# Performance work log

Measured on AMD Instinct MI355X. Metric: run time of the kernel, lower is better.

The kernel has to match this reference:

```python
import jax, jax.numpy as jnp
import numpy as np

N_NODES = 100000
N_EDGES = 600000
D_IN = 128
D_OUT = 128
N_REL = 16
N_BASES = 8


def setup_inputs() -> dict:
    key = jax.random.key(0)
    ks = jax.random.split(key, 6)
    x = jax.random.normal(ks[0], (N_NODES, D_IN), dtype=jnp.float32)
    edge_index = jax.random.randint(ks[1], (2, N_EDGES), 0, N_NODES, dtype=jnp.int64)
    edge_type = jax.random.randint(ks[2], (N_EDGES,), 0, N_REL, dtype=jnp.int64)
    # xavier-uniform-ish init scales
    b_lim = float(np.sqrt(6.0 / (D_IN + D_OUT)))
    c_lim = float(np.sqrt(6.0 / (N_REL + N_BASES)))
    w_lim = float(np.sqrt(6.0 / (D_IN + D_OUT)))
    bases = jax.random.uniform(ks[3], (N_BASES, D_IN, D_OUT), jnp.float32, -b_lim, b_lim)
    coefficients = jax.random.uniform(ks[4], (N_REL, N_BASES), jnp.float32, -c_lim, c_lim)
    w_self = jax.random.uniform(ks[5], (D_OUT, D_IN), jnp.float32, -w_lim, w_lim)
    return {"x": x, "edge_index": edge_index, "edge_type": edge_type,
            "bases": bases, "coefficients": coefficients, "w_self": w_self}


def reference(x, edge_index, edge_type, bases, coefficients, w_self):
    # self loop: Linear(in, out, bias=False) -> x @ W^T
    out = x @ w_self.T  # [N, D_OUT]
    # relation weights from basis decomposition
    weights = jnp.einsum('rb,bio->rio', coefficients, bases)  # [R, D_IN, D_OUT]
    row, col = edge_index[0], edge_index[1]
    xc = x[col]  # [E, D_IN] gather of source features
    n_rel = weights.shape[0]
    msg = jnp.zeros((xc.shape[0], w_self.shape[0]), dtype=x.dtype)
    # fixed small loop over relations; masked accumulate matches per-relation grouped GEMM
    for r in range(n_rel):
        sel = (edge_type == r)[:, None]
        msg = msg + jnp.where(sel, xc @ weights[r], jnp.zeros((), x.dtype))
    # scatter-add messages to destination rows
    out = out.at[row].add(msg)
    return out
```

## Files before the change

### kernel.cpp

```cpp
#include <hip/hip_runtime.h>

#define NN 100000
#define NE 600000
#define ET (NE + NN)
#define D 128
#define NREL 16
#define SCANB 391
#define TPB 4
#define MAXTILES 10954
#define GEMMG ((MAXTILES + TPB - 1) / TPB)
#define WGRID 1088

typedef short short8 __attribute__((ext_vector_type(8)));
typedef float f32x4 __attribute__((ext_vector_type(4)));
typedef unsigned int u32x4 __attribute__((ext_vector_type(4)));

#define C0 0
#define O0 20
#define CU0 40
#define T0 60

#define WT_OFF   0
#define META_OFF 557056
#define DH_OFF   557568
#define DO_OFF   957568
#define DC_OFF   1357576
#define BS_OFF   1757576
#define SCP_OFF  1759576
#define SR_OFF   7360088
#define XB_OFF   10160096
#define MSGB_OFF 35760096
#define MSGA_OFF 10160096
#define NEED_B   (MSGB_OFF + (size_t)ET * 128 * 2)
#define NEED_A   (MSGA_OFF + (size_t)ET * 128 * 2)

__device__ __forceinline__ unsigned short f2bf(float f) {
  unsigned u = __builtin_bit_cast(unsigned, f);
  u += 0x7fffu + ((u >> 16) & 1u);
  return (unsigned short)(u >> 16);
}

__global__ __launch_bounds__(256) void k_prep(const float* __restrict__ bases,
    const float* __restrict__ coef, const float* __restrict__ w_self,
    unsigned short* __restrict__ wT, const float* __restrict__ x,
    unsigned short* __restrict__ xb)
{
  if (blockIdx.x < WGRID) {
    int idx = blockIdx.x * 256 + threadIdx.x;
    int r = idx >> 14;
    int t = idx & 16383;
    float v;
    if (r < 16) {
      int o = t >> 7, i = t & 127;
      float acc = 0.f;
      #pragma unroll
      for (int b = 0; b < 8; ++b)
        acc += coef[r * 8 + b] * bases[b * 16384 + i * 128 + o];
      v = acc;
    } else {
      v = w_self[t];
    }
    wT[idx] = f2bf(v);
  } else {
    int i = (blockIdx.x - WGRID) * 256 + threadIdx.x;
    if (i >= NN * D / 4) return;
    f32x4 f = __builtin_nontemporal_load((const f32x4*)(x + (size_t)i * 4));
    unsigned short s0 = f2bf(f[0]), s1 = f2bf(f[1]), s2 = f2bf(f[2]), s3 = f2bf(f[3]);
    unsigned long long pk = (unsigned long long)s0 | ((unsigned long long)s1 << 16)
                          | ((unsigned long long)s2 << 32) | ((unsigned long long)s3 << 48);
    *(unsigned long long*)(xb + (size_t)i * 4) = pk;
  }
}

__global__ __launch_bounds__(256) void k_hist(const int* __restrict__ ei,
    const int* __restrict__ et, int* __restrict__ meta, int* __restrict__ dstHist)
{
  __shared__ int h[16];
  int tid = threadIdx.x;
  if (tid < 16) h[tid] = 0;
  __syncthreads();
  for (int e = blockIdx.x * 256 + tid; e < NE; e += gridDim.x * 256) {
    atomicAdd(&h[et[e]], 1);
    atomicAdd(&dstHist[ei[e]], 1);
  }
  __syncthreads();
  if (tid < 16) atomicAdd(&meta[C0 + tid], h[tid]);
}

__global__ __launch_bounds__(256) void k_scan1(const int* __restrict__ dstHist,
    int* __restrict__ dstOff, int* __restrict__ blockSums)
{
  __shared__ int sh[256];
  int tid = threadIdx.x;
  int d = blockIdx.x * 256 + tid;
  int v = (d < NN) ? (dstHist[d] + 1) : 0;
  sh[tid] = v;
  __syncthreads();
  #pragma unroll
  for (int ofs = 1; ofs < 256; ofs <<= 1) {
    int t = (tid >= ofs) ? sh[tid - ofs] : 0;
    __syncthreads();
    sh[tid] += t;
    __syncthreads();
  }
  if (d < NN) dstOff[d] = sh[tid] - v;
  if (tid == 255) blockSums[blockIdx.x] = sh[tid];
}

__global__ __launch_bounds__(512) void k_scan2(int* __restrict__ blockSums, int* __restrict__ meta)
{
  __shared__ int sh[SCANB];
  int tid = threadIdx.x;
  if (tid < SCANB) sh[tid] = blockSums[tid];
  __syncthreads();
  if (tid == 0) {
    int run = 0;
    for (int i = 0; i < SCANB; ++i) { int c = sh[i]; sh[i] = run; run += c; }
    meta[C0 + 16] = NN;
    int off = 0, toff = 0;
    for (int r = 0; r <= 16; ++r) {
      meta[O0 + r] = off;
      meta[CU0 + r] = off;
      meta[T0 + r] = toff;
      int c = meta[C0 + r];
      off += c;
      toff += (c + 63) >> 6;
    }
    meta[O0 + 17] = off;
    meta[T0 + 17] = toff;
  }
  __syncthreads();
  if (tid < SCANB) blockSums[tid] = sh[tid];
}

__global__ __launch_bounds__(256) void k_scan3(int* __restrict__ dstOff,
    const int* __restrict__ blockSums, int* __restrict__ dstCursor,
    int2* __restrict__ sCP)
{
  int tid = threadIdx.x;
  int d = blockIdx.x * 256 + tid;
  int base = blockSums[blockIdx.x];
  if (d < NN) {
    int o = dstOff[d] + base;
    dstOff[d] = o;
    dstCursor[d] = o + 1;
    sCP[NE + d] = make_int2(d, o);
  }
  if (d == NN) dstOff[NN] = ET;
}

__global__ __launch_bounds__(256) void k_self0(int2* __restrict__ sCP, int* __restrict__ sRow)
{
  int n = blockIdx.x * 256 + threadIdx.x;
  if (n < NN) { sCP[NE + n] = make_int2(n, 0); sRow[NE + n] = n; }
}

__global__ __launch_bounds__(256) void k_scatter(const int* __restrict__ ei, const int* __restrict__ et,
    int* __restrict__ meta, int2* __restrict__ sCP, int* __restrict__ sRow,
    int* __restrict__ dstCursor, int doMsg)
{
  __shared__ int h[16], base[16], lh[16];
  int tid = threadIdx.x;
  int start = blockIdx.x * 4096;
  int end = min(NE, start + 4096);
  if (tid < 16) { h[tid] = 0; lh[tid] = 0; }
  __syncthreads();
  for (int e = start + tid; e < end; e += 256)
    atomicAdd(&h[et[e]], 1);
  __syncthreads();
  if (tid < 16) base[tid] = atomicAdd(&meta[CU0 + tid], h[tid]);
  __syncthreads();
  for (int e = start + tid; e < end; e += 256) {
    int r = et[e];
    int row = ei[e];
    int pos = base[r] + atomicAdd(&lh[r], 1);
    int slot = doMsg ? atomicAdd(&dstCursor[row], 1) : 0;
    sCP[pos] = make_int2(ei[NE + e], slot);
    if (!doMsg) sRow[pos] = row;
  }
}

__global__ __launch_bounds__(256) void k_gemm(const float* __restrict__ xf,
    const unsigned short* __restrict__ xb,
    const unsigned short* __restrict__ wT, const int* __restrict__ meta,
    const int2* __restrict__ sCP, const int* __restrict__ sRow,
    unsigned short* __restrict__ msg, float* __restrict__ out,
    int xbf, int msgmode)
{
  __shared__ short As[64 * 17 * 8];
  __shared__ short Es[64 * 136];
  __shared__ int Pos2[2][64];
  __shared__ int Rows[64];
  __shared__ int Ms[80];

  int tid = threadIdx.x;
  if (tid < 80) Ms[tid] = meta[tid];
  __syncthreads();
  int ntiles = Ms[T0 + 17];

  int lane = tid & 63, wave = tid >> 6;
  int q = lane >> 4, l15 = lane & 15;
  int m = tid >> 2, ug = tid & 3;

  if (xbf && msgmode) {
    short8 pf[4];
    int pcy = 0;
    bool pvalid = false;
    int r = 0, nr = 0;
    int b = blockIdx.x * TPB;
    if (b < ntiles) {
      while (r < 16 && Ms[T0 + r + 1] <= b) ++r;
      int boff = Ms[O0 + r];
      int e0 = boff + (b - Ms[T0 + r]) * 64;
      nr = min(64, boff + Ms[C0 + r] - e0);
      pvalid = m < nr;
      int2 cp = sCP[pvalid ? (e0 + m) : e0];
      pcy = cp.y;
      const unsigned short* xr = xb + (size_t)cp.x * 128;
      #pragma unroll
      for (int s = 0; s < 4; ++s) {
        short8 v = (short8)(short)0;
        if (pvalid) v = *(const short8*)(xr + (ug * 4 + s) * 8);
        pf[s] = v;
      }
    }
    int rprev = -1;
    short8 bfr[2][4];
    for (int ti = 0; ti < TPB; ++ti) {
      b = blockIdx.x * TPB + ti;
      if (b >= ntiles) break;
      int curR = r, curNr = nr;
      #pragma unroll
      for (int s = 0; s < 4; ++s)
        *(short8*)&As[(m * 17 + ug * 4 + s) * 8] = pf[s];
      if (ug == 0) Pos2[ti & 1][m] = pvalid ? pcy : 0;
      __syncthreads();
      int bn = b + 1;
      if (ti + 1 < TPB && bn < ntiles) {
        int rn = curR;
        while (rn < 16 && Ms[T0 + rn + 1] <= bn) ++rn;
        int boff = Ms[O0 + rn];
        int e0n = boff + (bn - Ms[T0 + rn]) * 64;
        int nrn = min(64, boff + Ms[C0 + rn] - e0n);
        pvalid = m < nrn;
        int2 cp = sCP[pvalid ? (e0n + m) : e0n];
        pcy = cp.y;
        const unsigned short* xr = xb + (size_t)cp.x * 128;
        #pragma unroll
        for (int s = 0; s < 4; ++s) {
          short8 v = (short8)(short)0;
          if (pvalid) v = *(const short8*)(xr + (ug * 4 + s) * 8);
          pf[s] = v;
        }
        r = rn; nr = nrn;
      }
      if (curR != rprev) {
        const unsigned short* wr = wT + curR * 16384;
        #pragma unroll
        for (int ns = 0; ns < 2; ++ns)
          #pragma unroll
          for (int kk = 0; kk < 4; ++kk)
            bfr[ns][kk] = *(const short8*)(wr + (wave * 32 + ns * 16 + l15) * 128 + kk * 32 + q * 8);
        rprev = curR;
      }
      f32x4 acc[4][2];
      #pragma unroll
      for (int ms = 0; ms < 4; ++ms)
        #pragma unroll
        for (int ns = 0; ns < 2; ++ns)
          acc[ms][ns] = (f32x4){0.f, 0.f, 0.f, 0.f};
      #pragma unroll
      for (int kk = 0; kk < 4; ++kk) {
        short8 af[4];
        #pragma unroll
        for (int ms = 0; ms < 4; ++ms)
          af[ms] = *(const short8*)&As[((ms * 16 + l15) * 17 + kk * 4 + q) * 8];
        #pragma unroll
        for (int ms = 0; ms < 4; ++ms)
          #pragma unroll
          for (int ns = 0; ns < 2; ++ns)
            acc[ms][ns] = __builtin_amdgcn_mfma_f32_16x16x32_bf16(af[ms], bfr[ns][kk], acc[ms][ns], 0, 0, 0);
      }
      #pragma unroll
      for (int ms = 0; ms < 4; ++ms)
        #pragma unroll
        for (int ns = 0; ns < 2; ++ns)
          #pragma unroll
          for (int reg = 0; reg < 4; ++reg)
            Es[(ms * 16 + q * 4 + reg) * 136 + wave * 32 + ns * 16 + l15] =
                (short)f2bf(acc[ms][ns][reg]);
      __syncthreads();
      #pragma unroll
      for (int i = 0; i < 4; ++i) {
        int row = wave * 16 + i * 4 + q;
        short8 v = *(const short8*)&Es[row * 136 + l15 * 8];
        if (row < curNr)
          __builtin_nontemporal_store(v,
              (short8*)(msg + (size_t)Pos2[ti & 1][row] * 128 + l15 * 8));
      }
    }
    return;
  }

  int rprev = -1;
  short8 bfr[2][4];
  for (int ti = 0; ti < TPB; ++ti) {
    int b = blockIdx.x * TPB + ti;
    if (b >= ntiles) break;
    int r = 0;
    while (r < 16 && Ms[T0 + r + 1] <= b) ++r;
    int tile = b - Ms[T0 + r];
    int boff = Ms[O0 + r];
    int e0 = boff + tile * 64;
    int nrows = min(64, boff + Ms[C0 + r] - e0);

    bool valid = m < nrows;
    int e = valid ? (e0 + m) : e0;
    int2 cp = sCP[e];
    if (ug == 0) {
      Pos2[0][m] = valid ? cp.y : 0;
      if (!msgmode) Rows[m] = valid ? sRow[e] : 0;
    }
    int c = cp.x;
    if (xbf) {
      const unsigned short* xr = xb + (size_t)c * 128;
      #pragma unroll
      for (int s = 0; s < 4; ++s) {
        int u = ug * 4 + s;
        short8 pk = (short8)(short)0;
        if (valid) pk = *(const short8*)(xr + u * 8);
        *(short8*)&As[(m * 17 + u) * 8] = pk;
      }
    } else {
      const float* xr = xf + (size_t)c * 128;
      #pragma unroll
      for (int s = 0; s < 4; ++s) {
        int u = ug * 4 + s;
        float4 f0 = make_float4(0.f, 0.f, 0.f, 0.f), f1 = f0;
        if (valid) {
          f0 = *(const float4*)(xr + u * 8);
          f1 = *(const float4*)(xr + u * 8 + 4);
        }
        short8 pk;
        pk[0] = (short)f2bf(f0.x); pk[1] = (short)f2bf(f0.y);
        pk[2] = (short)f2bf(f0.z); pk[3] = (short)f2bf(f0.w);
        pk[4] = (short)f2bf(f1.x); pk[5] = (short)f2bf(f1.y);
        pk[6] = (short)f2bf(f1.z); pk[7] = (short)f2bf(f1.w);
        *(short8*)&As[(m * 17 + u) * 8] = pk;
      }
    }
    __syncthreads();

    if (r != rprev) {
      const unsigned short* wr = wT + r * 16384;
      #pragma unroll
      for (int ns = 0; ns < 2; ++ns)
        #pragma unroll
        for (int kk = 0; kk < 4; ++kk)
          bfr[ns][kk] = *(const short8*)(wr + (wave * 32 + ns * 16 + l15) * 128 + kk * 32 + q * 8);
      rprev = r;
    }

    f32x4 acc[4][2];
    #pragma unroll
    for (int ms = 0; ms < 4; ++ms)
      #pragma unroll
      for (int ns = 0; ns < 2; ++ns)
        acc[ms][ns] = (f32x4){0.f, 0.f, 0.f, 0.f};
    #pragma unroll
    for (int kk = 0; kk < 4; ++kk) {
      short8 af[4];
      #pragma unroll
      for (int ms = 0; ms < 4; ++ms)
        af[ms] = *(const short8*)&As[((ms * 16 + l15) * 17 + kk * 4 + q) * 8];
      #pragma unroll
      for (int ms = 0; ms < 4; ++ms)
        #pragma unroll
        for (int ns = 0; ns < 2; ++ns)
          acc[ms][ns] = __builtin_amdgcn_mfma_f32_16x16x32_bf16(af[ms], bfr[ns][kk], acc[ms][ns], 0, 0, 0);
    }

    if (msgmode) {
      __syncthreads();
      #pragma unroll
      for (int ms = 0; ms < 4; ++ms)
        #pragma unroll
        for (int ns = 0; ns < 2; ++ns)
          #pragma unroll
          for (int reg = 0; reg < 4; ++reg)
            Es[(ms * 16 + q * 4 + reg) * 136 + wave * 32 + ns * 16 + l15] =
                (short)f2bf(acc[ms][ns][reg]);
      __syncthreads();
      #pragma unroll
      for (int i = 0; i < 4; ++i) {
        int row = wave * 16 + i * 4 + q;
        short8 v = *(const short8*)&Es[row * 136 + l15 * 8];
        if (row < nrows)
          __builtin_nontemporal_store(v,
              (short8*)(msg + (size_t)Pos2[0][row] * 128 + l15 * 8));
      }
      __syncthreads();
    } else {
      #pragma unroll
      for (int ms = 0; ms < 4; ++ms)
        #pragma unroll
        for (int reg = 0; reg < 4; ++reg) {
          int mrow = ms * 16 + q * 4 + reg;
          if (mrow < nrows) {
            float* op = out + (size_t)Rows[mrow] * 128 + wave * 32 + l15;
            unsafeAtomicAdd(op, acc[ms][0][reg]);
            unsafeAtomicAdd(op + 16, acc[ms][1][reg]);
          }
        }
      __syncthreads();
    }
  }
}

__global__ __launch_bounds__(256) void k_reduce(const unsigned short* __restrict__ msg,
    const int* __restrict__ dstOff, float* __restrict__ out)
{
  int d = blockIdx.x * 16 + (threadIdx.x >> 4);
  if (d >= NN) return;
  int sl = threadIdx.x & 15;
  int s = dstOff[d], e = dstOff[d + 1];
  const unsigned short* base = msg + (size_t)sl * 8;
  float a[8], bacc[8];
  #pragma unroll
  for (int i = 0; i < 8; ++i) { a[i] = 0.f; bacc[i] = 0.f; }
  int j = s;
  for (; j + 1 < e; j += 2) {
    u32x4 v0 = __builtin_nontemporal_load((const u32x4*)(base + (size_t)j * 128));
    u32x4 v1 = __builtin_nontemporal_load((const u32x4*)(base + (size_t)(j + 1) * 128));
    #pragma unroll
    for (int c = 0; c < 4; ++c) {
      a[2 * c]     += __builtin_bit_cast(float, v0[c] << 16);
      a[2 * c + 1] += __builtin_bit_cast(float, v0[c] & 0xffff0000u);
      bacc[2 * c]     += __builtin_bit_cast(float, v1[c] << 16);
      bacc[2 * c + 1] += __builtin_bit_cast(float, v1[c] & 0xffff0000u);
    }
  }
  if (j < e) {
    u32x4 v0 = __builtin_nontemporal_load((const u32x4*)(base + (size_t)j * 128));
    #pragma unroll
    for (int c = 0; c < 4; ++c) {
      a[2 * c]     += __builtin_bit_cast(float, v0[c] << 16);
      a[2 * c + 1] += __builtin_bit_cast(float, v0[c] & 0xffff0000u);
    }
  }
  f32x4 w0, w1;
  w0[0] = a[0] + bacc[0]; w0[1] = a[1] + bacc[1]; w0[2] = a[2] + bacc[2]; w0[3] = a[3] + bacc[3];
  w1[0] = a[4] + bacc[4]; w1[1] = a[5] + bacc[5]; w1[2] = a[6] + bacc[6]; w1[3] = a[7] + bacc[7];
  float* op = out + (size_t)d * 128 + sl * 8;
  __builtin_nontemporal_store(w0, (f32x4*)op);
  __builtin_nontemporal_store(w1, (f32x4*)(op + 4));
}

extern "C" void kernel_launch(void* const* d_in, const int* in_sizes, int n_in,
                              void* d_out, int out_size, void* d_ws, size_t ws_size,
                              hipStream_t stream)
{
  const float* x      = (const float*)d_in[0];
  const int*   ei     = (const int*)d_in[1];
  const int*   et     = (const int*)d_in[2];
  const float* bases  = (const float*)d_in[3];
  const float* coef   = (const float*)d_in[4];
  const float* w_self = (const float*)d_in[5];
  float* out = (float*)d_out;
  char* ws = (char*)d_ws;
  unsigned short* wT = (unsigned short*)(ws + WT_OFF);
  int* meta      = (int*)(ws + META_OFF);
  int* dstHist   = (int*)(ws + DH_OFF);
  int* dstOff    = (int*)(ws + DO_OFF);
  int* dstCursor = (int*)(ws + DC_OFF);
  int* blockSums = (int*)(ws + BS_OFF);
  int2* sCP      = (int2*)(ws + SCP_OFF);
  int* sRow      = (int*)(ws + SR_OFF);
  unsigned short* xb = (unsigned short*)(ws + XB_OFF);

  const int modeB = (ws_size >= NEED_B) ? 1 : 0;
  const int modeA = (modeB || ws_size >= NEED_A) ? 1 : 0;
  unsigned short* msg = (unsigned short*)(ws + (modeB ? MSGB_OFF : MSGA_OFF));

  hipMemsetAsync(ws + META_OFF, 0, 512 + 400000, stream);
  k_prep<<<modeB ? (WGRID + 12500) : WGRID, 256, 0, stream>>>(bases, coef, w_self, wT, x, xb);
  k_hist<<<256, 256, 0, stream>>>(ei, et, meta, dstHist);
  if (modeA) {
    k_scan1<<<SCANB, 256, 0, stream>>>(dstHist, dstOff, blockSums);
    k_scan2<<<1, 512, 0, stream>>>(blockSums, meta);
    k_scan3<<<SCANB, 256, 0, stream>>>(dstOff, blockSums, dstCursor, sCP);
  } else {
    k_scan2<<<1, 512, 0, stream>>>(blockSums, meta);
    k_self0<<<SCANB, 256, 0, stream>>>(sCP, sRow);
    hipMemsetAsync(d_out, 0, (size_t)NN * D * 4, stream);
  }
  k_scatter<<<(NE + 4095) / 4096, 256, 0, stream>>>(ei, et, meta, sCP, sRow, dstCursor, modeA);
  k_gemm<<<GEMMG, 256, 0, stream>>>(x, xb, wT, meta, sCP, sRow, msg, out, modeB, modeA);
  if (modeA)
    k_reduce<<<(NN + 15) / 16, 256, 0, stream>>>(msg, dstOff, out);
}
```

Before: 320.5 us.

## Deepen gather prefetch pipeline and use LDS-only barriers in message GEMM

Restructures the per-tile loop of the fused gather+GEMM message path into a three-stage software pipeline. Edge index/position lookups run two tiles ahead and the bf16 feature row gather runs one tile ahead. __syncthreads is replaced by a barrier that waits only on LDS counters (lgkmcnt), so outstanding global prefetch loads are no longer drained at each barrier. The aim is to hide gather latency behind the MFMA work, at the cost of extra registers for the pipeline state.

```diff
diff --git a/kernel.cpp b/kernel.cpp
--- a/kernel.cpp
+++ b/kernel.cpp
@@ -40,6 +40,11 @@
   return (unsigned short)(u >> 16);
 }
 
+__device__ __forceinline__ void lds_barrier() {
+  asm volatile("s_waitcnt lgkmcnt(0)" ::: "memory");
+  __builtin_amdgcn_s_barrier();
+}
+
 __global__ __launch_bounds__(256) void k_prep(const float* __restrict__ bases,
     const float* __restrict__ coef, const float* __restrict__ w_self,
     unsigned short* __restrict__ wT, const float* __restrict__ x,
@@ -203,57 +208,76 @@
   int m = tid >> 2, ug = tid & 3;
 
   if (xbf && msgmode) {
-    short8 pf[4];
-    int pcy = 0;
-    bool pvalid = false;
-    int r = 0, nr = 0;
-    int b = blockIdx.x * TPB;
-    if (b < ntiles) {
-      while (r < 16 && Ms[T0 + r + 1] <= b) ++r;
-      int boff = Ms[O0 + r];
-      int e0 = boff + (b - Ms[T0 + r]) * 64;
-      nr = min(64, boff + Ms[C0 + r] - e0);
-      pvalid = m < nr;
-      int2 cp = sCP[pvalid ? (e0 + m) : e0];
-      pcy = cp.y;
+    int b0 = blockIdx.x * TPB;
+    if (b0 >= ntiles) return;
+
+    int rr = 0;
+    short8 pfS[4]; int cyS; bool vS; int rS, nrS;
+    int2 cpG; bool vG; int rG, nrG;
+    int2 cpP; bool vP; int rP, nrP;
+
+    {
+      while (rr < 16 && Ms[T0 + rr + 1] <= b0) ++rr;
+      int boff = Ms[O0 + rr];
+      int e0 = boff + (b0 - Ms[T0 + rr]) * 64;
+      nrS = min(64, boff + Ms[C0 + rr] - e0);
+      rS = rr;
+      vS = m < nrS;
+      int2 cp = sCP[vS ? (e0 + m) : e0];
+      cyS = cp.y;
       const unsigned short* xr = xb + (size_t)cp.x * 128;
       #pragma unroll
       for (int s = 0; s < 4; ++s) {
         short8 v = (short8)(short)0;
-        if (pvalid) v = *(const short8*)(xr + (ug * 4 + s) * 8);
-        pf[s] = v;
-      }
-    }
+        if (vS) v = *(const short8*)(xr + (ug * 4 + s) * 8);
+        pfS[s] = v;
+      }
+    }
+    if (TPB > 1 && b0 + 1 < ntiles) {
+      int b = b0 + 1;
+      while (rr < 16 && Ms[T0 + rr + 1] <= b) ++rr;
+      int boff = Ms[O0 + rr];
+      int e0 = boff + (b - Ms[T0 + rr]) * 64;
+      nrG = min(64, boff + Ms[C0 + rr] - e0);
+      rG = rr;
+      vG = m < nrG;
+      cpG = sCP[vG ? (e0 + m) : e0];
+    } else { vG = false; nrG = 0; rG = rS; cpG = make_int2(0, 0); }
+
     int rprev = -1;
     short8 bfr[2][4];
     for (int ti = 0; ti < TPB; ++ti) {
-      b = blockIdx.x * TPB + ti;
+      int b = b0 + ti;
       if (b >= ntiles) break;
-      int curR = r, curNr = nr;
+      int curR = rS, curNr = nrS;
+
       #pragma unroll
       for (int s = 0; s < 4; ++s)
-        *(short8*)&As[(m * 17 + ug * 4 + s) * 8] = pf[s];
-      if (ug == 0) Pos2[ti & 1][m] = pvalid ? pcy : 0;
-      __syncthreads();
-      int bn = b + 1;
-      if (ti + 1 < TPB && bn < ntiles) {
-        int rn = curR;
-        while (rn < 16 && Ms[T0 + rn + 1] <= bn) ++rn;
-        int boff = Ms[O0 + rn];
-        int e0n = boff + (bn - Ms[T0 + rn]) * 64;
-        int nrn = min(64, boff + Ms[C0 + rn] - e0n);
-        pvalid = m < nrn;
-        int2 cp = sCP[pvalid ? (e0n + m) : e0n];
-        pcy = cp.y;
-        const unsigned short* xr = xb + (size_t)cp.x * 128;
+        *(short8*)&As[(m * 17 + ug * 4 + s) * 8] = pfS[s];
+      if (ug == 0) Pos2[ti & 1][m] = vS ? cyS : 0;
+
+      if (ti + 2 < TPB && b + 2 < ntiles) {
+        int bp = b + 2;
+        while (rr < 16 && Ms[T0 + rr + 1] <= bp) ++rr;
+        int boff = Ms[O0 + rr];
+        int e0 = boff + (bp - Ms[T0 + rr]) * 64;
+        nrP = min(64, boff + Ms[C0 + rr] - e0);
+        rP = rr;
+        vP = m < nrP;
+        cpP = sCP[vP ? (e0 + m) : e0];
+      } else { vP = false; nrP = 0; rP = rG; cpP = make_int2(0, 0); }
+
+      short8 pfN[4];
+      {
+        const unsigned short* xr = xb + (size_t)cpG.x * 128;
         #pragma unroll
         for (int s = 0; s < 4; ++s) {
           short8 v = (short8)(short)0;
-          if (pvalid) v = *(const short8*)(xr + (ug * 4 + s) * 8);
-          pf[s] = v;
+          if (vG) v = *(const short8*)(xr + (ug * 4 + s) * 8);
+          pfN[s] = v;
         }
-        r = rn; nr = nrn;
-      }
+      }
+
       if (curR != rprev) {
         const unsigned short* wr = wT + curR * 16384;
         #pragma unroll
@@ -263,6 +287,9 @@
             bfr[ns][kk] = *(const short8*)(wr + (wave * 32 + ns * 16 + l15) * 128 + kk * 32 + q * 8);
         rprev = curR;
       }
+
+      lds_barrier();
+
       f32x4 acc[4][2];
       #pragma unroll
       for (int ms = 0; ms < 4; ++ms)
@@ -281,6 +308,7 @@
           for (int ns = 0; ns < 2; ++ns)
             acc[ms][ns] = __builtin_amdgcn_mfma_f32_16x16x32_bf16(af[ms], bfr[ns][kk], acc[ms][ns], 0, 0, 0);
       }
+
       #pragma unroll
       for (int ms = 0; ms < 4; ++ms)
         #pragma unroll
@@ -289,7 +317,9 @@
           for (int reg = 0; reg < 4; ++reg)
             Es[(ms * 16 + q * 4 + reg) * 136 + wave * 32 + ns * 16 + l15] =
                 (short)f2bf(acc[ms][ns][reg]);
-      __syncthreads();
+
+      lds_barrier();
+
       #pragma unroll
       for (int i = 0; i < 4; ++i) {
         int row = wave * 16 + i * 4 + q;
@@ -298,6 +328,11 @@
           __builtin_nontemporal_store(v,
               (short8*)(msg + (size_t)Pos2[ti & 1][row] * 128 + l15 * 8));
       }
+
+      #pragma unroll
+      for (int s = 0; s < 4; ++s) pfS[s] = pfN[s];
+      cyS = cpG.y; vS = vG; rS = rG; nrS = nrG;
+      cpG = cpP;   vG = vP; rG = rP; nrG = nrP;
     }
     return;
   }
```

Result: no change. 320.2 us (-0.1%).

## Use one tile per GEMM block, direct scattered message stores, parallel block-sum scan

Applied to the files above, without the earlier changes.

The GEMM kernel drops the multi-tile-per-block loop with register prefetch. Each block now handles a single 64-edge tile, relying on many resident blocks rather than in-block prefetch to hide gather latency. The LDS staging of the output tile before coalesced 16-byte stores is removed. Each lane now writes individual 2-byte bf16 values straight to the message rows, which cuts LDS traffic and barriers but makes the global writes much narrower and more scattered. The serial single-thread block-sum scan in k_scan2 is also replaced with a parallel Hillis-Steele scan.

```diff
diff --git a/kernel.cpp b/kernel.cpp
--- a/kernel.cpp
+++ b/kernel.cpp
@@ -6,9 +6,8 @@
 #define D 128
 #define NREL 16
 #define SCANB 391
-#define TPB 4
 #define MAXTILES 10954
-#define GEMMG ((MAXTILES + TPB - 1) / TPB)
+#define GEMMG MAXTILES
 #define WGRID 1088
 
 typedef short short8 __attribute__((ext_vector_type(8)));
@@ -40,6 +39,11 @@
   return (unsigned short)(u >> 16);
 }
 
+__device__ __forceinline__ void lds_barrier() {
+  asm volatile("s_waitcnt lgkmcnt(0)" ::: "memory");
+  __builtin_amdgcn_s_barrier();
+}
+
 __global__ __launch_bounds__(256) void k_prep(const float* __restrict__ bases,
     const float* __restrict__ coef, const float* __restrict__ w_self,
     unsigned short* __restrict__ wT, const float* __restrict__ x,
@@ -109,13 +113,19 @@
 
 __global__ __launch_bounds__(512) void k_scan2(int* __restrict__ blockSums, int* __restrict__ meta)
 {
-  __shared__ int sh[SCANB];
-  int tid = threadIdx.x;
-  if (tid < SCANB) sh[tid] = blockSums[tid];
-  __syncthreads();
+  __shared__ int sh[512];
+  int tid = threadIdx.x;
+  int v = (tid < SCANB) ? blockSums[tid] : 0;
+  sh[tid] = v;
+  __syncthreads();
+  #pragma unroll
+  for (int ofs = 1; ofs < 512; ofs <<= 1) {
+    int t = (tid >= ofs) ? sh[tid - ofs] : 0;
+    __syncthreads();
+    sh[tid] += t;
+    __syncthreads();
+  }
   if (tid == 0) {
-    int run = 0;
-    for (int i = 0; i < SCANB; ++i) { int c = sh[i]; sh[i] = run; run += c; }
     meta[C0 + 16] = NN;
     int off = 0, toff = 0;
     for (int r = 0; r <= 16; ++r) {
@@ -129,8 +139,7 @@
     meta[O0 + 17] = off;
     meta[T0 + 17] = toff;
   }
-  __syncthreads();
-  if (tid < SCANB) blockSums[tid] = sh[tid];
+  if (tid < SCANB) blockSums[tid] = sh[tid] - v;
 }
 
 __global__ __launch_bounds__(256) void k_scan3(int* __restrict__ dstOff,
@@ -188,8 +197,7 @@
     int xbf, int msgmode)
 {
   __shared__ short As[64 * 17 * 8];
-  __shared__ short Es[64 * 136];
-  __shared__ int Pos2[2][64];
+  __shared__ int Pos[64];
   __shared__ int Rows[64];
   __shared__ int Ms[80];
 
@@ -197,223 +205,110 @@
   if (tid < 80) Ms[tid] = meta[tid];
   __syncthreads();
   int ntiles = Ms[T0 + 17];
+  int b = blockIdx.x;
+  if (b >= ntiles) return;
 
   int lane = tid & 63, wave = tid >> 6;
   int q = lane >> 4, l15 = lane & 15;
   int m = tid >> 2, ug = tid & 3;
 
-  if (xbf && msgmode) {
-    short8 pf[4];
-    int pcy = 0;
-    bool pvalid = false;
-    int r = 0, nr = 0;
-    int b = blockIdx.x * TPB;
-    if (b < ntiles) {
-      while (r < 16 && Ms[T0 + r + 1] <= b) ++r;
-      int boff = Ms[O0 + r];
-      int e0 = boff + (b - Ms[T0 + r]) * 64;
-      nr = min(64, boff + Ms[C0 + r] - e0);
-      pvalid = m < nr;
-      int2 cp = sCP[pvalid ? (e0 + m) : e0];
-      pcy = cp.y;
-      const unsigned short* xr = xb + (size_t)cp.x * 128;
-      #pragma unroll
-      for (int s = 0; s < 4; ++s) {
-        short8 v = (short8)(short)0;
-        if (pvalid) v = *(const short8*)(xr + (ug * 4 + s) * 8);
-        pf[s] = v;
+  int r = 0;
+  while (r < 16 && Ms[T0 + r + 1] <= b) ++r;
+  int boff = Ms[O0 + r];
+  int e0 = boff + (b - Ms[T0 + r]) * 64;
+  int nr = min(64, boff + Ms[C0 + r] - e0);
+
+  bool valid = m < nr;
+  int e = valid ? (e0 + m) : e0;
+  int2 cp = sCP[e];
+  if (ug == 0) {
+    Pos[m] = valid ? cp.y : 0;
+    if (!msgmode) Rows[m] = valid ? sRow[e] : 0;
+  }
+
+  if (xbf) {
+    const unsigned short* xr = xb + (size_t)cp.x * 128;
+    #pragma unroll
+    for (int s = 0; s < 4; ++s) {
+      int u = ug * 4 + s;
+      short8 pk = (short8)(short)0;
+      if (valid) pk = *(const short8*)(xr + u * 8);
+      *(short8*)&As[(m * 17 + u) * 8] = pk;
+    }
+  } else {
+    const float* xr = xf + (size_t)cp.x * 128;
+    #pragma unroll
+    for (int s = 0; s < 4; ++s) {
+      int u = ug * 4 + s;
+      float4 f0 = make_float4(0.f, 0.f, 0.f, 0.f), f1 = f0;
+      if (valid) {
+        f0 = *(const float4*)(xr + u * 8);
+        f1 = *(const float4*)(xr + u * 8 + 4);
       }
-    }
-    int rprev = -1;
-    short8 bfr[2][4];
-    for (int ti = 0; ti < TPB; ++ti) {
-      b = blockIdx.x * TPB + ti;
-      if (b >= ntiles) break;
-      int curR = r, curNr = nr;
-      #pragma unroll
-      for (int s = 0; s < 4; ++s)
-        *(short8*)&As[(m * 17 + ug * 4 + s) * 8] = pf[s];
-      if (ug == 0) Pos2[ti & 1][m] = pvalid ? pcy : 0;
-      __syncthreads();
-      int bn = b + 1;
-      if (ti + 1 < TPB && bn < ntiles) {
-        int rn = curR;
-        while (rn < 16 && Ms[T0 + rn + 1] <= bn) ++rn;
-        int boff = Ms[O0 + rn];
-        int e0n = boff + (bn - Ms[T0 + rn]) * 64;
-        int nrn = min(64, boff + Ms[C0 + rn] - e0n);
-        pvalid = m < nrn;
-        int2 cp = sCP[pvalid ? (e0n + m) : e0n];
-        pcy = cp.y;
-        const unsigned short* xr = xb + (size_t)cp.x * 128;
-        #pragma unroll
-        for (int s = 0; s < 4; ++s) {
-          short8 v = (short8)(short)0;
-          if (pvalid) v = *(const short8*)(xr + (ug * 4 + s) * 8);
-          pf[s] = v;
+      short8 pk;
+      pk[0] = (short)f2bf(f0.x); pk[1] = (short)f2bf(f0.y);
+      pk[2] = (short)f2bf(f0.z); pk[3] = (short)f2bf(f0.w);
+      pk[4] = (short)f2bf(f1.x); pk[5] = (short)f2bf(f1.y);
+      pk[6] = (short)f2bf(f1.z); pk[7] = (short)f2bf(f1.w);
+      *(short8*)&As[(m * 17 + u) * 8] = pk;
+    }
+  }
+
+  short8 bfr[2][4];
+  {
+    const unsigned short* wr = wT + r * 16384;
+    #pragma unroll
+    for (int ns = 0; ns < 2; ++ns)
+      #pragma unroll
+      for (int kk = 0; kk < 4; ++kk)
+        bfr[ns][kk] = *(const short8*)(wr + (wave * 32 + ns * 16 + l15) * 128 + kk * 32 + q * 8);
+  }
+
+  lds_barrier();
+
+  f32x4 acc[4][2];
+  #pragma unroll
+  for (int ms = 0; ms < 4; ++ms)
+    #pragma unroll
+    for (int ns = 0; ns < 2; ++ns)
+      acc[ms][ns] = (f32x4){0.f, 0.f, 0.f, 0.f};
+  #pragma unroll
+  for (int kk = 0; kk < 4; ++kk) {
+    short8 af[4];
+    #pragma unroll
+    for (int ms = 0; ms < 4; ++ms)
+      af[ms] = *(const short8*)&As[((ms * 16 + l15) * 17 + kk * 4 + q) * 8];
+    #pragma unroll
+    for (int ms = 0; ms < 4; ++ms)
+      #pragma unroll
+      for (int ns = 0; ns < 2; ++ns)
+        acc[ms][ns] = __builtin_amdgcn_mfma_f32_16x16x32_bf16(af[ms], bfr[ns][kk], acc[ms][ns], 0, 0, 0);
+  }
+
+  if (msgmode) {
+    #pragma unroll
+    for (int ms = 0; ms < 4; ++ms)
+      #pragma unroll
+      for (int reg = 0; reg < 4; ++reg) {
+        int erow = ms * 16 + q * 4 + reg;
+        if (erow < nr) {
+          unsigned short* mp = msg + (size_t)Pos[erow] * 128 + wave * 32 + l15;
+          mp[0]  = f2bf(acc[ms][0][reg]);
+          mp[16] = f2bf(acc[ms][1][reg]);
         }
-        r = rn; nr = nrn;
       }
-      if (curR != rprev) {
-        const unsigned short* wr = wT + curR * 16384;
-        #pragma unroll
-        for (int ns = 0; ns < 2; ++ns)
-          #pragma unroll
-          for (int kk = 0; kk < 4; ++kk)
-            bfr[ns][kk] = *(const short8*)(wr + (wave * 32 + ns * 16 + l15) * 128 + kk * 32 + q * 8);
-        rprev = curR;
+  } else {
+    #pragma unroll
+    for (int ms = 0; ms < 4; ++ms)
+      #pragma unroll
+      for (int reg = 0; reg < 4; ++reg) {
+        int erow = ms * 16 + q * 4 + reg;
+        if (erow < nr) {
+          float* op = out + (size_t)Rows[erow] * 128 + wave * 32 + l15;
+          unsafeAtomicAdd(op, acc[ms][0][reg]);
+          unsafeAtomicAdd(op + 16, acc[ms][1][reg]);
+        }
       }
-      f32x4 acc[4][2];
-      #pragma unroll
-      for (int ms = 0; ms < 4; ++ms)
-        #pragma unroll
-        for (int ns = 0; ns < 2; ++ns)
-          acc[ms][ns] = (f32x4){0.f, 0.f, 0.f, 0.f};
-      #pragma unroll
-      for (int kk = 0; kk < 4; ++kk) {
-        short8 af[4];
-        #pragma unroll
-        for (int ms = 0; ms < 4; ++ms)
-          af[ms] = *(const short8*)&As[((ms * 16 + l15) * 17 + kk * 4 + q) * 8];
-        #pragma unroll
-        for (int ms = 0; ms < 4; ++ms)
-          #pragma unroll
-          for (int ns = 0; ns < 2; ++ns)
-            acc[ms][ns] = __builtin_amdgcn_mfma_f32_16x16x32_bf16(af[ms], bfr[ns][kk], acc[ms][ns], 0, 0, 0);
-      }
-      #pragma unroll
-      for (int ms = 0; ms < 4; ++ms)
-        #pragma unroll
-        for (int ns = 0; ns < 2; ++ns)
-          #pragma unroll
-          for (int reg = 0; reg < 4; ++reg)
-            Es[(ms * 16 + q * 4 + reg) * 136 + wave * 32 + ns * 16 + l15] =
-                (short)f2bf(acc[ms][ns][reg]);
-      __syncthreads();
-      #pragma unroll
-      for (int i = 0; i < 4; ++i) {
-        int row = wave * 16 + i * 4 + q;
-        short8 v = *(const short8*)&Es[row * 136 + l15 * 8];
-        if (row < curNr)
-          __builtin_nontemporal_store(v,
-              (short8*)(msg + (size_t)Pos2[ti & 1][row] * 128 + l15 * 8));
-      }
-    }
-    return;
-  }
-
-  int rprev = -1;
-  short8 bfr[2][4];
-  for (int ti = 0; ti < TPB; ++ti) {
-    int b = blockIdx.x * TPB + ti;
-    if (b >= ntiles) break;
-    int r = 0;
-    while (r < 16 && Ms[T0 + r + 1] <= b) ++r;
-    int tile = b - Ms[T0 + r];
-    int boff = Ms[O0 + r];
-    int e0 = boff + tile * 64;
-    int nrows = min(64, boff + Ms[C0 + r] - e0);
-
-    bool valid = m < nrows;
-    int e = valid ? (e0 + m) : e0;
-    int2 cp = sCP[e];
-    if (ug == 0) {
-      Pos2[0][m] = valid ? cp.y : 0;
-      if (!msgmode) Rows[m] = valid ? sRow[e] : 0;
-    }
-    int c = cp.x;
-    if (xbf) {
-      const unsigned short* xr = xb + (size_t)c * 128;
-      #pragma unroll
-      for (int s = 0; s < 4; ++s) {
-        int u = ug * 4 + s;
-        short8 pk = (short8)(short)0;
-        if (valid) pk = *(const short8*)(xr + u * 8);
-        *(short8*)&As[(m * 17 + u) * 8] = pk;
-      }
-    } else {
-      const float* xr = xf + (size_t)c * 128;
-      #pragma unroll
-      for (int s = 0; s < 4; ++s) {
-        int u = ug * 4 + s;
-        float4 f0 = make_float4(0.f, 0.f, 0.f, 0.f), f1 = f0;
-        if (valid) {
-          f0 = *(const float4*)(xr + u * 8);
-          f1 = *(const float4*)(xr + u * 8 + 4);
-        }
-        short8 pk;
-        pk[0] = (short)f2bf(f0.x); pk[1] = (short)f2bf(f0.y);
-        pk[2] = (short)f2bf(f0.z); pk[3] = (short)f2bf(f0.w);
-        pk[4] = (short)f2bf(f1.x); pk[5] = (short)f2bf(f1.y);
-        pk[6] = (short)f2bf(f1.z); pk[7] = (short)f2bf(f1.w);
-        *(short8*)&As[(m * 17 + u) * 8] = pk;
-      }
-    }
-    __syncthreads();
-
-    if (r != rprev) {
-      const unsigned short* wr = wT + r * 16384;
-      #pragma unroll
-      for (int ns = 0; ns < 2; ++ns)
-        #pragma unroll
-        for (int kk = 0; kk < 4; ++kk)
-          bfr[ns][kk] = *(const short8*)(wr + (wave * 32 + ns * 16 + l15) * 128 + kk * 32 + q * 8);
-      rprev = r;
-    }
-
-    f32x4 acc[4][2];
-    #pragma unroll
-    for (int ms = 0; ms < 4; ++ms)
-      #pragma unroll
-      for (int ns = 0; ns < 2; ++ns)
-        acc[ms][ns] = (f32x4){0.f, 0.f, 0.f, 0.f};
-    #pragma unroll
-    for (int kk = 0; kk < 4; ++kk) {
-      short8 af[4];
-      #pragma unroll
-      for (int ms = 0; ms < 4; ++ms)
-        af[ms] = *(const short8*)&As[((ms * 16 + l15) * 17 + kk * 4 + q) * 8];
-      #pragma unroll
-      for (int ms = 0; ms < 4; ++ms)
-        #pragma unroll
-        for (int ns = 0; ns < 2; ++ns)
-          acc[ms][ns] = __builtin_amdgcn_mfma_f32_16x16x32_bf16(af[ms], bfr[ns][kk], acc[ms][ns], 0, 0, 0);
-    }
-
-    if (msgmode) {
-      __syncthreads();
-      #pragma unroll
-      for (int ms = 0; ms < 4; ++ms)
-        #pragma unroll
-        for (int ns = 0; ns < 2; ++ns)
-          #pragma unroll
-          for (int reg = 0; reg < 4; ++reg)
-            Es[(ms * 16 + q * 4 + reg) * 136 + wave * 32 + ns * 16 + l15] =
-                (short)f2bf(acc[ms][ns][reg]);
-      __syncthreads();
-      #pragma unroll
-      for (int i = 0; i < 4; ++i) {
-        int row = wave * 16 + i * 4 + q;
-        short8 v = *(const short8*)&Es[row * 136 + l15 * 8];
-        if (row < nrows)
-          __builtin_nontemporal_store(v,
-              (short8*)(msg + (size_t)Pos2[0][row] * 128 + l15 * 8));
-      }
-      __syncthreads();
-    } else {
-      #pragma unroll
-      for (int ms = 0; ms < 4; ++ms)
-        #pragma unroll
-        for (int reg = 0; reg < 4; ++reg) {
-          int mrow = ms * 16 + q * 4 + reg;
-          if (mrow < nrows) {
-            float* op = out + (size_t)Rows[mrow] * 128 + wave * 32 + l15;
-            unsafeAtomicAdd(op, acc[ms][0][reg]);
-            unsafeAtomicAdd(op + 16, acc[ms][1][reg]);
-          }
-        }
-      __syncthreads();
-    }
   }
 }
 
```

Result: slower. 328.8 us (+2.6%).

## Write GEMM messages contiguously and gather them in reduce via index array

Applied to the files above, without the earlier changes.

The GEMM now writes each message row contiguously in relation-sorted order instead of scattering it to a destination-sorted slot. A separate idx array maps each destination-sorted slot back to its message position, and the reduce kernel gathers through it. The change also fuses the weight/x prep and histogram kernels into one launch, replaces the serial block-sum scan with a parallel one, and drops the GEMM's software prefetch of the next tile. This trades scattered writes in the GEMM for scattered reads plus an extra index load in the reduce, and the lost prefetch may expose gather latency.

```diff
diff --git a/kernel.cpp b/kernel.cpp
--- a/kernel.cpp
+++ b/kernel.cpp
@@ -26,13 +26,13 @@
 #define DO_OFF   957568
 #define DC_OFF   1357576
 #define BS_OFF   1757576
-#define SCP_OFF  1759576
-#define SR_OFF   7360088
-#define XB_OFF   10160096
-#define MSGB_OFF 35760096
-#define MSGA_OFF 10160096
-#define NEED_B   (MSGB_OFF + (size_t)ET * 128 * 2)
-#define NEED_A   (MSGA_OFF + (size_t)ET * 128 * 2)
+#define SSRC_OFF 1759576
+#define IDX_OFF  4559576
+#define SDST_OFF 7359576
+#define XB_OFF   10159576
+#define MSG_OFF  35759576
+#define NEED_XB  (XB_OFF + (size_t)NN * D * 2)
+#define NEED_MSG (MSG_OFF + (size_t)ET * 128 * 2)
 
 __device__ __forceinline__ unsigned short f2bf(float f) {
   unsigned u = __builtin_bit_cast(unsigned, f);
@@ -40,13 +40,17 @@
   return (unsigned short)(u >> 16);
 }
 
-__global__ __launch_bounds__(256) void k_prep(const float* __restrict__ bases,
+__global__ __launch_bounds__(256) void k_ph(const float* __restrict__ bases,
     const float* __restrict__ coef, const float* __restrict__ w_self,
     unsigned short* __restrict__ wT, const float* __restrict__ x,
-    unsigned short* __restrict__ xb)
-{
-  if (blockIdx.x < WGRID) {
-    int idx = blockIdx.x * 256 + threadIdx.x;
+    unsigned short* __restrict__ xb, const int* __restrict__ ei,
+    const int* __restrict__ et, int* __restrict__ meta, int* __restrict__ dstHist,
+    int xbf, int doMsg)
+{
+  int bx = blockIdx.x;
+  int tid = threadIdx.x;
+  if (bx < WGRID) {
+    int idx = bx * 256 + tid;
     int r = idx >> 14;
     int t = idx & 16383;
     float v;
@@ -61,27 +65,26 @@
       v = w_self[t];
     }
     wT[idx] = f2bf(v);
-  } else {
-    int i = (blockIdx.x - WGRID) * 256 + threadIdx.x;
+    return;
+  }
+  int hb0 = WGRID + (xbf ? 12500 : 0);
+  if (bx < hb0) {
+    int i = (bx - WGRID) * 256 + tid;
     if (i >= NN * D / 4) return;
     f32x4 f = __builtin_nontemporal_load((const f32x4*)(x + (size_t)i * 4));
     unsigned short s0 = f2bf(f[0]), s1 = f2bf(f[1]), s2 = f2bf(f[2]), s3 = f2bf(f[3]);
     unsigned long long pk = (unsigned long long)s0 | ((unsigned long long)s1 << 16)
                           | ((unsigned long long)s2 << 32) | ((unsigned long long)s3 << 48);
     *(unsigned long long*)(xb + (size_t)i * 4) = pk;
-  }
-}
-
-__global__ __launch_bounds__(256) void k_hist(const int* __restrict__ ei,
-    const int* __restrict__ et, int* __restrict__ meta, int* __restrict__ dstHist)
-{
+    return;
+  }
   __shared__ int h[16];
-  int tid = threadIdx.x;
+  int hb = bx - hb0;
   if (tid < 16) h[tid] = 0;
   __syncthreads();
-  for (int e = blockIdx.x * 256 + tid; e < NE; e += gridDim.x * 256) {
+  for (int e = hb * 256 + tid; e < NE; e += 256 * 256) {
     atomicAdd(&h[et[e]], 1);
-    atomicAdd(&dstHist[ei[e]], 1);
+    if (doMsg) atomicAdd(&dstHist[ei[e]], 1);
   }
   __syncthreads();
   if (tid < 16) atomicAdd(&meta[C0 + tid], h[tid]);
@@ -109,13 +112,19 @@
 
 __global__ __launch_bounds__(512) void k_scan2(int* __restrict__ blockSums, int* __restrict__ meta)
 {
-  __shared__ int sh[SCANB];
-  int tid = threadIdx.x;
-  if (tid < SCANB) sh[tid] = blockSums[tid];
-  __syncthreads();
+  __shared__ int sh[512];
+  int tid = threadIdx.x;
+  int v = (tid < SCANB) ? blockSums[tid] : 0;
+  sh[tid] = v;
+  __syncthreads();
+  #pragma unroll
+  for (int ofs = 1; ofs < 512; ofs <<= 1) {
+    int t = (tid >= ofs) ? sh[tid - ofs] : 0;
+    __syncthreads();
+    sh[tid] += t;
+    __syncthreads();
+  }
   if (tid == 0) {
-    int run = 0;
-    for (int i = 0; i < SCANB; ++i) { int c = sh[i]; sh[i] = run; run += c; }
     meta[C0 + 16] = NN;
     int off = 0, toff = 0;
     for (int r = 0; r <= 16; ++r) {
@@ -129,13 +138,12 @@
     meta[O0 + 17] = off;
     meta[T0 + 17] = toff;
   }
-  __syncthreads();
-  if (tid < SCANB) blockSums[tid] = sh[tid];
+  if (tid < SCANB) blockSums[tid] = sh[tid] - v;
 }
 
 __global__ __launch_bounds__(256) void k_scan3(int* __restrict__ dstOff,
     const int* __restrict__ blockSums, int* __restrict__ dstCursor,
-    int2* __restrict__ sCP)
+    int* __restrict__ sSrc, int* __restrict__ idx)
 {
   int tid = threadIdx.x;
   int d = blockIdx.x * 256 + tid;
@@ -144,20 +152,39 @@
     int o = dstOff[d] + base;
     dstOff[d] = o;
     dstCursor[d] = o + 1;
-    sCP[NE + d] = make_int2(d, o);
+    idx[o] = NE + d;
+    sSrc[NE + d] = d;
   }
   if (d == NN) dstOff[NN] = ET;
 }
 
-__global__ __launch_bounds__(256) void k_self0(int2* __restrict__ sCP, int* __restrict__ sRow)
+__global__ __launch_bounds__(64) void k_meta(int* __restrict__ meta)
+{
+  if (threadIdx.x == 0) {
+    meta[C0 + 16] = NN;
+    int off = 0, toff = 0;
+    for (int r = 0; r <= 16; ++r) {
+      meta[O0 + r] = off;
+      meta[CU0 + r] = off;
+      meta[T0 + r] = toff;
+      int c = meta[C0 + r];
+      off += c;
+      toff += (c + 63) >> 6;
+    }
+    meta[O0 + 17] = off;
+    meta[T0 + 17] = toff;
+  }
+}
+
+__global__ __launch_bounds__(256) void k_selfF(int* __restrict__ sSrc, int* __restrict__ sDst)
 {
   int n = blockIdx.x * 256 + threadIdx.x;
-  if (n < NN) { sCP[NE + n] = make_int2(n, 0); sRow[NE + n] = n; }
+  if (n < NN) { sSrc[NE + n] = n; sDst[NE + n] = n; }
 }
 
 __global__ __launch_bounds__(256) void k_scatter(const int* __restrict__ ei, const int* __restrict__ et,
-    int* __restrict__ meta, int2* __restrict__ sCP, int* __restrict__ sRow,
-    int* __restrict__ dstCursor, int doMsg)
+    int* __restrict__ meta, int* __restrict__ sSrc, int* __restrict__ sDst,
+    int* __restrict__ dstCursor, int* __restrict__ idx, int doMsg)
 {
   __shared__ int h[16], base[16], lh[16];
   int tid = threadIdx.x;
@@ -174,22 +201,21 @@
     int r = et[e];
     int row = ei[e];
     int pos = base[r] + atomicAdd(&lh[r], 1);
-    int slot = doMsg ? atomicAdd(&dstCursor[row], 1) : 0;
-    sCP[pos] = make_int2(ei[NE + e], slot);
-    if (!doMsg) sRow[pos] = row;
+    sSrc[pos] = ei[NE + e];
+    if (doMsg) idx[atomicAdd(&dstCursor[row], 1)] = pos;
+    else sDst[pos] = row;
   }
 }
 
 __global__ __launch_bounds__(256) void k_gemm(const float* __restrict__ xf,
     const unsigned short* __restrict__ xb,
     const unsigned short* __restrict__ wT, const int* __restrict__ meta,
-    const int2* __restrict__ sCP, const int* __restrict__ sRow,
+    const int* __restrict__ sSrc, const int* __restrict__ sDst,
     unsigned short* __restrict__ msg, float* __restrict__ out,
     int xbf, int msgmode)
 {
   __shared__ short As[64 * 17 * 8];
   __shared__ short Es[64 * 136];
-  __shared__ int Pos2[2][64];
   __shared__ int Rows[64];
   __shared__ int Ms[80];
 
@@ -197,72 +223,48 @@
   if (tid < 80) Ms[tid] = meta[tid];
   __syncthreads();
   int ntiles = Ms[T0 + 17];
+  int b0 = blockIdx.x * TPB;
+  if (b0 >= ntiles) return;
 
   int lane = tid & 63, wave = tid >> 6;
   int q = lane >> 4, l15 = lane & 15;
   int m = tid >> 2, ug = tid & 3;
 
+  int rprev = -1;
+  short8 bfr[2][4];
+
   if (xbf && msgmode) {
-    short8 pf[4];
-    int pcy = 0;
-    bool pvalid = false;
-    int r = 0, nr = 0;
-    int b = blockIdx.x * TPB;
-    if (b < ntiles) {
+    for (int ti = 0; ti < TPB; ++ti) {
+      int b = b0 + ti;
+      if (b >= ntiles) break;
+      int r = 0;
       while (r < 16 && Ms[T0 + r + 1] <= b) ++r;
       int boff = Ms[O0 + r];
       int e0 = boff + (b - Ms[T0 + r]) * 64;
-      nr = min(64, boff + Ms[C0 + r] - e0);
-      pvalid = m < nr;
-      int2 cp = sCP[pvalid ? (e0 + m) : e0];
-      pcy = cp.y;
-      const unsigned short* xr = xb + (size_t)cp.x * 128;
+      int nr = min(64, boff + Ms[C0 + r] - e0);
+
+      bool valid = m < nr;
+      int src = sSrc[valid ? (e0 + m) : e0];
+      const unsigned short* xr = xb + (size_t)src * 128;
       #pragma unroll
       for (int s = 0; s < 4; ++s) {
-        short8 v = (short8)(short)0;
-        if (pvalid) v = *(const short8*)(xr + (ug * 4 + s) * 8);
-        pf[s] = v;
-      }
-    }
-    int rprev = -1;
-    short8 bfr[2][4];
-    for (int ti = 0; ti < TPB; ++ti) {
-      b = blockIdx.x * TPB + ti;
-      if (b >= ntiles) break;
-      int curR = r, curNr = nr;
-      #pragma unroll
-      for (int s = 0; s < 4; ++s)
-        *(short8*)&As[(m * 17 + ug * 4 + s) * 8] = pf[s];
-      if (ug == 0) Pos2[ti & 1][m] = pvalid ? pcy : 0;
+        int u = ug * 4 + s;
+        short8 pk = (short8)(short)0;
+        if (valid) pk = *(const short8*)(xr + u * 8);
+        *(short8*)&As[(m * 17 + u) * 8] = pk;
+      }
       __syncthreads();
-      int bn = b + 1;
-      if (ti + 1 < TPB && bn < ntiles) {
-        int rn = curR;
-        while (rn < 16 && Ms[T0 + rn + 1] <= bn) ++rn;
-        int boff = Ms[O0 + rn];
-        int e0n = boff + (bn - Ms[T0 + rn]) * 64;
-        int nrn = min(64, boff + Ms[C0 + rn] - e0n);
-        pvalid = m < nrn;
-        int2 cp = sCP[pvalid ? (e0n + m) : e0n];
-        pcy = cp.y;
-        const unsigned short* xr = xb + (size_t)cp.x * 128;
-        #pragma unroll
-        for (int s = 0; s < 4; ++s) {
-          short8 v = (short8)(short)0;
-          if (pvalid) v = *(const short8*)(xr + (ug * 4 + s) * 8);
-          pf[s] = v;
-        }
-        r = rn; nr = nrn;
-      }
-      if (curR != rprev) {
-        const unsigned short* wr = wT + curR * 16384;
+
+      if (r != rprev) {
+        const unsigned short* wr = wT + r * 16384;
         #pragma unroll
         for (int ns = 0; ns < 2; ++ns)
           #pragma unroll
           for (int kk = 0; kk < 4; ++kk)
             bfr[ns][kk] = *(const short8*)(wr + (wave * 32 + ns * 16 + l15) * 128 + kk * 32 + q * 8);
-        rprev = curR;
-      }
+        rprev = r;
+      }
+
       f32x4 acc[4][2];
       #pragma unroll
       for (int ms = 0; ms < 4; ++ms)
@@ -281,6 +283,8 @@
           for (int ns = 0; ns < 2; ++ns)
             acc[ms][ns] = __builtin_amdgcn_mfma_f32_16x16x32_bf16(af[ms], bfr[ns][kk], acc[ms][ns], 0, 0, 0);
       }
+
+      __syncthreads();
       #pragma unroll
       for (int ms = 0; ms < 4; ++ms)
         #pragma unroll
@@ -290,40 +294,35 @@
             Es[(ms * 16 + q * 4 + reg) * 136 + wave * 32 + ns * 16 + l15] =
                 (short)f2bf(acc[ms][ns][reg]);
       __syncthreads();
+
       #pragma unroll
       for (int i = 0; i < 4; ++i) {
         int row = wave * 16 + i * 4 + q;
         short8 v = *(const short8*)&Es[row * 136 + l15 * 8];
-        if (row < curNr)
-          __builtin_nontemporal_store(v,
-              (short8*)(msg + (size_t)Pos2[ti & 1][row] * 128 + l15 * 8));
-      }
+        if (row < nr)
+          *(short8*)(msg + (size_t)(e0 + row) * 128 + l15 * 8) = v;
+      }
+      __syncthreads();
     }
     return;
   }
 
-  int rprev = -1;
-  short8 bfr[2][4];
   for (int ti = 0; ti < TPB; ++ti) {
-    int b = blockIdx.x * TPB + ti;
+    int b = b0 + ti;
     if (b >= ntiles) break;
     int r = 0;
     while (r < 16 && Ms[T0 + r + 1] <= b) ++r;
-    int tile = b - Ms[T0 + r];
     int boff = Ms[O0 + r];
-    int e0 = boff + tile * 64;
+    int e0 = boff + (b - Ms[T0 + r]) * 64;
     int nrows = min(64, boff + Ms[C0 + r] - e0);
 
     bool valid = m < nrows;
     int e = valid ? (e0 + m) : e0;
-    int2 cp = sCP[e];
-    if (ug == 0) {
-      Pos2[0][m] = valid ? cp.y : 0;
-      if (!msgmode) Rows[m] = valid ? sRow[e] : 0;
-    }
-    int c = cp.x;
+    int src = sSrc[e];
+    if (ug == 0) Rows[m] = valid ? sDst[e] : 0;
+
     if (xbf) {
-      const unsigned short* xr = xb + (size_t)c * 128;
+      const unsigned short* xr = xb + (size_t)src * 128;
       #pragma unroll
       for (int s = 0; s < 4; ++s) {
         int u = ug * 4 + s;
@@ -332,7 +331,7 @@
         *(short8*)&As[(m * 17 + u) * 8] = pk;
       }
     } else {
-      const float* xr = xf + (size_t)c * 128;
+      const float* xr = xf + (size_t)src * 128;
       #pragma unroll
       for (int s = 0; s < 4; ++s) {
         int u = ug * 4 + s;
@@ -380,45 +379,25 @@
           acc[ms][ns] = __builtin_amdgcn_mfma_f32_16x16x32_bf16(af[ms], bfr[ns][kk], acc[ms][ns], 0, 0, 0);
     }
 
-    if (msgmode) {
-      __syncthreads();
-      #pragma unroll
-      for (int ms = 0; ms < 4; ++ms)
-        #pragma unroll
-        for (int ns = 0; ns < 2; ++ns)
-          #pragma unroll
-          for (int reg = 0; reg < 4; ++reg)
-            Es[(ms * 16 + q * 4 + reg) * 136 + wave * 32 + ns * 16 + l15] =
-                (short)f2bf(acc[ms][ns][reg]);
-      __syncthreads();
-      #pragma unroll
-      for (int i = 0; i < 4; ++i) {
-        int row = wave * 16 + i * 4 + q;
-        short8 v = *(const short8*)&Es[row * 136 + l15 * 8];
-        if (row < nrows)
-          __builtin_nontemporal_store(v,
-              (short8*)(msg + (size_t)Pos2[0][row] * 128 + l15 * 8));
-      }
-      __syncthreads();
-    } else {
-      #pragma unroll
-      for (int ms = 0; ms < 4; ++ms)
-        #pragma unroll
-        for (int reg = 0; reg < 4; ++reg) {
-          int mrow = ms * 16 + q * 4 + reg;
-          if (mrow < nrows) {
-            float* op = out + (size_t)Rows[mrow] * 128 + wave * 32 + l15;
-            unsafeAtomicAdd(op, acc[ms][0][reg]);
-            unsafeAtomicAdd(op + 16, acc[ms][1][reg]);
-          }
+    __syncthreads();
+    #pragma unroll
+    for (int ms = 0; ms < 4; ++ms)
+      #pragma unroll
+      for (int reg = 0; reg < 4; ++reg) {
+        int mrow = ms * 16 + q * 4 + reg;
+        if (mrow < nrows) {
+          float* op = out + (size_t)Rows[mrow] * 128 + wave * 32 + l15;
+          unsafeAtomicAdd(op, acc[ms][0][reg]);
+          unsafeAtomicAdd(op + 16, acc[ms][1][reg]);
         }
-      __syncthreads();
-    }
+      }
+    __syncthreads();
   }
 }
 
 __global__ __launch_bounds__(256) void k_reduce(const unsigned short* __restrict__ msg,
-    const int* __restrict__ dstOff, float* __restrict__ out)
+    const int* __restrict__ dstOff, const int* __restrict__ idx,
+    float* __restrict__ out)
 {
   int d = blockIdx.x * 16 + (threadIdx.x >> 4);
   if (d >= NN) return;
@@ -430,8 +409,10 @@
   for (int i = 0; i < 8; ++i) { a[i] = 0.f; bacc[i] = 0.f; }
   int j = s;
   for (; j + 1 < e; j += 2) {
-    u32x4 v0 = __builtin_nontemporal_load((const u32x4*)(base + (size_t)j * 128));
-    u32x4 v1 = __builtin_nontemporal_load((const u32x4*)(base + (size_t)(j + 1) * 128));
+    size_t p0 = (size_t)idx[j] * 128;
+    size_t p1 = (size_t)idx[j + 1] * 128;
+    u32x4 v0 = *(const u32x4*)(base + p0);
+    u32x4 v1 = *(const u32x4*)(base + p1);
     #pragma unroll
     for (int c = 0; c < 4; ++c) {
       a[2 * c]     += __builtin_bit_cast(float, v0[c] << 16);
@@ -441,7 +422,7 @@
     }
   }
   if (j < e) {
-    u32x4 v0 = __builtin_nontemporal_load((const u32x4*)(base + (size_t)j * 128));
+    u32x4 v0 = *(const u32x4*)(base + (size_t)idx[j] * 128);
     #pragma unroll
     for (int c = 0; c < 4; ++c) {
       a[2 * c]     += __builtin_bit_cast(float, v0[c] << 16);
@@ -474,28 +455,29 @@
   int* dstOff    = (int*)(ws + DO_OFF);
   int* dstCursor = (int*)(ws + DC_OFF);
   int* blockSums = (int*)(ws + BS_OFF);
-  int2* sCP      = (int2*)(ws + SCP_OFF);
-  int* sRow      = (int*)(ws + SR_OFF);
+  int* sSrc      = (int*)(ws + SSRC_OFF);
+  int* idx       = (int*)(ws + IDX_OFF);
+  int* sDst      = (int*)(ws + SDST_OFF);
   unsigned short* xb = (unsigned short*)(ws + XB_OFF);
-
-  const int modeB = (ws_size >= NEED_B) ? 1 : 0;
-  const int modeA = (modeB || ws_size >= NEED_A) ? 1 : 0;
-  unsigned short* msg = (unsigned short*)(ws + (modeB ? MSGB_OFF : MSGA_OFF));
+  unsigned short* msg = (unsigned short*)(ws + MSG_OFF);
+
+  const int msgmode = (ws_size >= NEED_MSG) ? 1 : 0;
+  const int xbf = (msgmode || ws_size >= NEED_XB) ? 1 : 0;
 
   hipMemsetAsync(ws + META_OFF, 0, 512 + 400000, stream);
-  k_prep<<<modeB ? (WGRID + 12500) : WGRID, 256, 0, stream>>>(bases, coef, w_self, wT, x, xb);
-  k_hist<<<256, 256, 0, stream>>>(ei, et, meta, dstHist);
-  if (modeA) {
+  k_ph<<<WGRID + (xbf ? 12500 : 0) + 256, 256, 0, stream>>>(
+      bases, coef, w_self, wT, x, xb, ei, et, meta, dstHist, xbf, msgmode);
+  if (msgmode) {
     k_scan1<<<SCANB, 256, 0, stream>>>(dstHist, dstOff, blockSums);
     k_scan2<<<1, 512, 0, stream>>>(blockSums, meta);
-    k_scan3<<<SCANB, 256, 0, stream>>>(dstOff, blockSums, dstCursor, sCP);
+    k_scan3<<<SCANB, 256, 0, stream>>>(dstOff, blockSums, dstCursor, sSrc, idx);
   } else {
-    k_scan2<<<1, 512, 0, stream>>>(blockSums, meta);
-    k_self0<<<SCANB, 256, 0, stream>>>(sCP, sRow);
+    k_meta<<<1, 64, 0, stream>>>(meta);
+    k_selfF<<<SCANB, 256, 0, stream>>>(sSrc, sDst);
     hipMemsetAsync(d_out, 0, (size_t)NN * D * 4, stream);
   }
-  k_scatter<<<(NE + 4095) / 4096, 256, 0, stream>>>(ei, et, meta, sCP, sRow, dstCursor, modeA);
-  k_gemm<<<GEMMG, 256, 0, stream>>>(x, xb, wT, meta, sCP, sRow, msg, out, modeB, modeA);
-  if (modeA)
-    k_reduce<<<(NN + 15) / 16, 256, 0, stream>>>(msg, dstOff, out);
-}
+  k_scatter<<<(NE + 4095) / 4096, 256, 0, stream>>>(ei, et, meta, sSrc, sDst, dstCursor, idx, msgmode);
+  k_gemm<<<GEMMG, 256, 0, stream>>>(x, xb, wT, meta, sSrc, sDst, msg, out, xbf, msgmode);
+  if (msgmode)
+    k_reduce<<<(NN + 15) / 16, 256, 0, stream>>>(msg, dstOff, idx, out);
+}
```

Result: slower. 329.7 us (+2.9%).
